# Optimization experiments

Measured on AMD Instinct MI355X. Metric: run time of the kernel, lower is better.

Reference implementation:

```python
import jax, jax.numpy as jnp
from jax import lax
import numpy as np

N_SEG = 8
C_IN = 256
C_RED = C_IN // 16
FOLD = C_IN // 8
EPS = 1e-5


def setup_inputs() -> dict:
    key = jax.random.key(0)
    ks = jax.random.split(key, 6)
    x = jax.random.normal(ks[0], (128, C_IN, 28, 28), dtype=jnp.float32)
    # ta_shift depthwise conv1d weight [C, 3], near one-hot init (learnable)
    w = np.zeros((C_IN, 3), dtype=np.float32)
    w[:FOLD, 2] = 1.0          # shift left (future)
    w[FOLD:2 * FOLD, 0] = 1.0  # shift right (past)
    w[2 * FOLD:, 1] = 1.0      # identity
    ta_shift_w = jnp.asarray(w)
    se_conv_w = jax.random.normal(ks[1], (C_RED, C_IN, 3), dtype=jnp.float32) * (1.0 / np.sqrt(3 * C_IN))
    bn_gamma = jnp.ones((C_RED,), dtype=jnp.float32)
    bn_beta = jnp.zeros((C_RED,), dtype=jnp.float32)
    se_conv1_w = jax.random.normal(ks[2], (C_IN, C_RED), dtype=jnp.float32) * (1.0 / np.sqrt(C_RED))
    net_w = jax.random.normal(ks[3], (C_IN, C_IN, 3, 3), dtype=jnp.float32) * (1.0 / np.sqrt(9 * C_IN))
    net_b = jnp.zeros((C_IN,), dtype=jnp.float32)
    return {"x": x, "ta_shift_w": ta_shift_w, "se_conv_w": se_conv_w,
            "bn_gamma": bn_gamma, "bn_beta": bn_beta, "se_conv1_w": se_conv1_w,
            "net_w": net_w, "net_b": net_b}


def reference(x, ta_shift_w, se_conv_w, bn_gamma, bn_beta, se_conv1_w, net_w, net_b):
    NT, C, H, W = x.shape
    T = N_SEG
    B = NT // T
    # --- temporal shift: depthwise conv1d (k=3, pad=1) over the segment axis ---
    x5 = x.reshape(B, T, C, H, W)
    xp = jnp.pad(x5, ((0, 0), (1, 1), (0, 0), (0, 0), (0, 0)))
    w0 = ta_shift_w[:, 0][None, None, :, None, None]
    w1 = ta_shift_w[:, 1][None, None, :, None, None]
    w2 = ta_shift_w[:, 2][None, None, :, None, None]
    xs = w0 * xp[:, :-2] + w1 * xp[:, 1:-1] + w2 * xp[:, 2:]  # [B,T,C,H,W]
    x_shift = xs.reshape(NT, C, H, W)
    # --- SE-style gating over pooled features ---
    y = x_shift.mean(axis=(2, 3))          # [NT, C]
    # faithful to torch: .view(-1, c, n_segment) reinterprets memory row-major
    y = y.reshape(B, C, T)                 # [B, C, T]
    y = lax.conv_general_dilated(y, se_conv_w, window_strides=(1,),
                                 padding=((1, 1),),
                                 dimension_numbers=("NCH", "OIH", "NCH"))  # [B, C/16, T]
    # BatchNorm1d (training-mode batch statistics over (N, L) per channel)
    mean = y.mean(axis=(0, 2), keepdims=True)
    var = ((y - mean) ** 2).mean(axis=(0, 2), keepdims=True)
    y = (y - mean) * lax.rsqrt(var + EPS)
    y = y * bn_gamma[None, :, None] + bn_beta[None, :, None]
    y = jax.nn.relu(y)
    y = jnp.einsum("oc,bct->bot", se_conv1_w, y)  # 1x1 conv, [B, C, T]
    y = jax.nn.sigmoid(y)
    y = y.reshape(NT, C, 1, 1)             # faithful row-major view back
    z = x_shift + x_shift * y
    # --- wrapped dense conv (self.net) ---
    out = lax.conv_general_dilated(z, net_w, window_strides=(1, 1),
                                   padding=((1, 1), (1, 1)),
                                   dimension_numbers=("NCHW", "OIHW", "NCHW"))
    out = out + net_b[None, :, None, None]
    return out
```

## Files before the change

### kernel.cpp

```cpp
#include <hip/hip_runtime.h>
#include <hip/hip_bf16.h>

typedef unsigned short u16;
typedef short bf16x8 __attribute__((ext_vector_type(8)));
typedef float f32x4 __attribute__((ext_vector_type(4)));
typedef unsigned short u16x8 __attribute__((ext_vector_type(8)));
typedef unsigned short u16x4 __attribute__((ext_vector_type(4)));

#define HW 784
#define PLANE 200704
#define PADPX 900

#define OFF_PX   0
#define OFF_Y3   131072
#define OFF_GL   262144
#define OFF_WT   393216
#define OFF_XSTG 1572864

__device__ __forceinline__ u16 f2b(float f) {
    union { float f; unsigned u; } v; v.f = f;
    unsigned r = v.u + 0x7FFF + ((v.u >> 16) & 1);
    return (u16)(r >> 16);
}

typedef __attribute__((address_space(1))) const unsigned int gas_u32;
typedef __attribute__((address_space(3))) unsigned int las_u32;
__device__ __forceinline__ void gload16(const void* g, void* l) {
    __builtin_amdgcn_global_load_lds((gas_u32*)g, (las_u32*)l, 16, 0, 0);
}

__global__ __launch_bounds__(256) void k_prep(const float* __restrict__ netw, u16* __restrict__ wt,
                                              u16* __restrict__ xstg,
                                              const float* __restrict__ x, float* __restrict__ px) {
    const int bx = blockIdx.x, tid = threadIdx.x;
    if (bx < 2304) {
        int id = bx * 256 + tid;
        int cl = id & 31, co = (id >> 5) & 255, cb = (id >> 13) & 7, tap = id >> 16;
        int ci = cb * 32 + cl;
        wt[id] = f2b(netw[((size_t)co * 256 + ci) * 9 + tap]);
    } else if (bx < 2432) {
        const int nt = bx - 2304;
        for (int it = 0; it < 15; ++it) {
            int cid = it * 256 + tid;
            if (cid < 3712) {
                int pxi = cid >> 5, ch = cid & 31;
                int pidx;
                if (pxi < 30) pidx = pxi;
                else if (pxi < 60) pidx = 29 * 30 + (pxi - 30);
                else { int k = pxi - 60; pidx = (1 + (k >> 1)) * 30 + (k & 1) * 29; }
                *(u16x8*)(xstg + ((size_t)nt * PADPX + pidx) * 256 + ch * 8) = (u16x8){0,0,0,0,0,0,0,0};
            }
        }
    } else {
        const int idx = bx - 2432;
        const int nt = idx >> 2, cg = idx & 3;
        const int wv = tid >> 6, ln = tid & 63;
        for (int i = 0; i < 16; ++i) {
            int c = cg * 64 + wv * 16 + i;
            const float4* xp = (const float4*)(x + (size_t)nt * PLANE + (size_t)c * HW);
            float s = 0.f;
            for (int k = ln; k < 196; k += 64) { float4 v = xp[k]; s += v.x + v.y + v.z + v.w; }
            #pragma unroll
            for (int o = 32; o; o >>= 1) s += __shfl_xor(s, o);
            if (ln == 0) px[nt * 256 + c] = s * (1.f / 784.f);
        }
    }
}

__global__ __launch_bounds__(256) void k_sea(const float* __restrict__ px,
                                             const float* __restrict__ taw,
                                             const float* __restrict__ wse,
                                             float* __restrict__ y3) {
    const int b = blockIdx.x, tid = threadIdx.x;
    __shared__ float ps_l[2048];
    __shared__ float part[2][128];
    #pragma unroll
    for (int i = 0; i < 8; ++i) {
        int e = i * 256 + tid;
        int ts = e >> 8, c = e & 255;
        int nt = b * 8 + ts;
        float v = taw[c * 3 + 1] * px[nt * 256 + c];
        if (ts > 0) v += taw[c * 3] * px[(nt - 1) * 256 + c];
        if (ts < 7) v += taw[c * 3 + 2] * px[(nt + 1) * 256 + c];
        ps_l[e] = v;
    }
    __syncthreads();
    const int half = tid >> 7;
    const int o = (tid & 127) >> 3, t = tid & 7;
    float acc = 0.f;
    const int c2a = half * 128;
    for (int c2 = c2a; c2 < c2a + 128; ++c2) {
        float w0 = wse[(o * 256 + c2) * 3];
        float w1 = wse[(o * 256 + c2) * 3 + 1];
        float w2 = wse[(o * 256 + c2) * 3 + 2];
        float v = w1 * ps_l[c2 * 8 + t];
        if (t > 0) v += w0 * ps_l[c2 * 8 + t - 1];
        if (t < 7) v += w2 * ps_l[c2 * 8 + t + 1];
        acc += v;
    }
    part[half][o * 8 + t] = acc;
    __syncthreads();
    if (tid < 128) y3[b * 128 + tid] = part[0][tid] + part[1][tid];
}

__global__ __launch_bounds__(256) void k_seb(const float* __restrict__ y3,
                                             const float* __restrict__ gamma,
                                             const float* __restrict__ beta,
                                             const float* __restrict__ w1,
                                             float* __restrict__ gl) {
    const int b = blockIdx.x, tid = threadIdx.x;
    __shared__ float y3_l[2048];
    __shared__ float sc[16], bi[16];
    __shared__ float yb[128];
    for (int i = tid; i < 2048; i += 256) y3_l[i] = y3[i];
    __syncthreads();
    if (tid < 16) {
        float s = 0.f, sq = 0.f;
        for (int i = 0; i < 128; ++i) {
            float v = y3_l[(i >> 3) * 128 + tid * 8 + (i & 7)];
            s += v; sq += v * v;
        }
        float m = s * (1.f / 128.f);
        float var = sq * (1.f / 128.f) - m * m;
        float rs = rsqrtf(var + 1e-5f) * gamma[tid];
        sc[tid] = rs; bi[tid] = beta[tid] - m * rs;
    }
    __syncthreads();
    if (tid < 128) {
        int oo = tid >> 3;
        yb[tid] = fmaxf(y3_l[b * 128 + tid] * sc[oo] + bi[oo], 0.f);
    }
    __syncthreads();
    float w1r[16];
    #pragma unroll
    for (int oo = 0; oo < 16; ++oo) w1r[oo] = w1[tid * 16 + oo];
    #pragma unroll
    for (int t = 0; t < 8; ++t) {
        float a = 0.f;
        #pragma unroll
        for (int oo = 0; oo < 16; ++oo) a += w1r[oo] * yb[oo * 8 + t];
        gl[b * 2048 + tid * 8 + t] = 1.f + 1.f / (1.f + __expf(-a));
    }
}

__global__ __launch_bounds__(256) void k_fused(const float* __restrict__ x,
                                               const float* __restrict__ taw,
                                               const float* __restrict__ gl,
                                               u16* __restrict__ xstg) {
    const int pt = blockIdx.x;
    const int nt = blockIdx.y;
    const int tid = threadIdx.x, wv = tid >> 6, ln = tid & 63;
    const int p0 = pt * 56;
    const int tseg = nt & 7;
    __shared__ float taw_l[768];
    __shared__ float gl_l[256];
    __shared__ __align__(16) u16 xs_l[256 * 60];
    for (int i = tid; i < 768; i += 256) taw_l[i] = taw[i];
    gl_l[tid] = gl[nt * 256 + tid];
    __syncthreads();
    const int g = ln >> 4;
    const int l = ln & 15;
    const bool act = l < 14;
    for (int j = 0; j < 16; ++j) {
        const int c = j * 16 + wv * 4 + g;
        const float w0 = taw_l[c * 3], w1 = taw_l[c * 3 + 1], w2 = taw_l[c * 3 + 2];
        const float gc = gl_l[c];
        const float* xb = x + (size_t)nt * PLANE + (size_t)c * HW + p0;
        float4 v0 = {0, 0, 0, 0}, vm = {0, 0, 0, 0}, vp = {0, 0, 0, 0};
        if (act) {
            v0 = *(const float4*)(xb + l * 4);
            if (w0 != 0.f && tseg > 0) vm = *(const float4*)(xb - PLANE + l * 4);
            if (w2 != 0.f && tseg < 7) vp = *(const float4*)(xb + PLANE + l * 4);
        }
        u16x4 o;
        o[0] = f2b((w0 * vm.x + w1 * v0.x + w2 * vp.x) * gc);
        o[1] = f2b((w0 * vm.y + w1 * v0.y + w2 * vp.y) * gc);
        o[2] = f2b((w0 * vm.z + w1 * v0.z + w2 * vp.z) * gc);
        o[3] = f2b((w0 * vm.w + w1 * v0.w + w2 * vp.w) * gc);
        if (act) *(u16x4*)&xs_l[c * 60 + l * 4] = o;
    }
    __syncthreads();
    for (int k = 0; k < 7; ++k) {
        int id = k * 256 + tid;
        int pp = id >> 5;
        int c0 = (id & 31) * 8;
        u16x8 v;
        #pragma unroll
        for (int i = 0; i < 8; ++i) v[i] = xs_l[(c0 + i) * 60 + pp];
        int gp = p0 + pp;
        int r = gp / 28, cc = gp % 28;
        int pidx = (r + 1) * 30 + (cc + 1);
        *(u16x8*)(xstg + ((size_t)nt * PADPX + pidx) * 256 + c0) = v;
    }
}

__global__ __launch_bounds__(256, 3) void k_conv(const u16* __restrict__ xstg,
                                                 const u16* __restrict__ wt,
                                                 const float* __restrict__ netb,
                                                 float* __restrict__ out) {
    const int pt = blockIdx.x;
    const int mt = blockIdx.y;
    const int nt = blockIdx.z;
    const int tid = threadIdx.x, wv = tid >> 6, ln = tid & 63;
    __shared__ __align__(16) u16 z_l[2][6144];
    const int qg = ln >> 4;
    const int p = ln & 15;
    const int g8 = qg * 8;
    int pb[7];
    #pragma unroll
    for (int nf = 0; nf < 7; ++nf) {
        int n = nf * 16 + p;
        pb[nf] = (n / 28) * 30 + (n % 28);
    }
    f32x4 acc[2][7];
    #pragma unroll
    for (int a = 0; a < 2; ++a)
        #pragma unroll
        for (int b = 0; b < 7; ++b) acc[a][b] = (f32x4){0.f, 0.f, 0.f, 0.f};

    const size_t gbase = ((size_t)nt * PADPX + pt * 120) * 256;
    const int maxpix = 899 - pt * 120;
    int pixl[3], ql[3];
    #pragma unroll
    for (int s = 0; s < 3; ++s) {
        int chunk = (wv * 3 + s) * 64 + ln;
        int px_ = chunk >> 2;
        ql[s] = chunk & 3;
        pixl[s] = px_ < maxpix ? px_ : maxpix;
    }

    auto stage = [&](int cb, int buf) {
        #pragma unroll
        for (int s = 0; s < 3; ++s) {
            const u16* g = xstg + gbase + (size_t)pixl[s] * 256 + cb * 32 + ql[s] * 8;
            gload16(g, &z_l[buf][(wv * 3 + s) * 512]);
        }
    };
    auto aload = [&](int tap, int cb, bf16x8* af) {
        const u16* ab = wt + (((size_t)tap * 8 + cb) * 256 + mt * 128 + wv * 32) * 32;
        af[0] = *(const bf16x8*)(ab + p * 32 + g8);
        af[1] = *(const bf16x8*)(ab + (16 + p) * 32 + g8);
    };

    bf16x8 afc[2], afn[2];
    aload(0, 0, afc);
    stage(0, 0);
    for (int cb = 0; cb < 8; ++cb) {
        asm volatile("s_waitcnt vmcnt(0)");
        __syncthreads();
        if (cb < 7) stage(cb + 1, (cb + 1) & 1);
        const u16* zl = z_l[cb & 1];
        #pragma unroll
        for (int tap = 0; tap < 9; ++tap) {
            if (tap < 8) aload(tap + 1, cb, afn);
            else if (cb < 7) aload(0, cb + 1, afn);
            const int po = (tap / 3) * 30 + (tap % 3);
            #pragma unroll
            for (int nf = 0; nf < 7; ++nf) {
                bf16x8 bf = *(const bf16x8*)&zl[(pb[nf] + po) * 32 + g8];
                acc[0][nf] = __builtin_amdgcn_mfma_f32_16x16x32_bf16(afc[0], bf, acc[0][nf], 0, 0, 0);
                acc[1][nf] = __builtin_amdgcn_mfma_f32_16x16x32_bf16(afc[1], bf, acc[1][nf], 0, 0, 0);
            }
            afc[0] = afn[0]; afc[1] = afn[1];
        }
    }
    const int colp = ln & 15, rowp = (ln >> 4) * 4;
    const int o0 = pt * 112;
    #pragma unroll
    for (int mf = 0; mf < 2; ++mf) {
        #pragma unroll
        for (int i = 0; i < 4; ++i) {
            int co = mt * 128 + wv * 32 + mf * 16 + rowp + i;
            float bias = netb[co];
            float* ob = out + ((size_t)nt * 256 + co) * HW + o0;
            #pragma unroll
            for (int nf = 0; nf < 7; ++nf)
                ob[nf * 16 + colp] = acc[mf][nf][i] + bias;
        }
    }
}

extern "C" void kernel_launch(void* const* d_in, const int* in_sizes, int n_in,
                              void* d_out, int out_size, void* d_ws, size_t ws_size,
                              hipStream_t stream) {
    const float* x     = (const float*)d_in[0];
    const float* taw   = (const float*)d_in[1];
    const float* wse   = (const float*)d_in[2];
    const float* gamma = (const float*)d_in[3];
    const float* beta  = (const float*)d_in[4];
    const float* w1    = (const float*)d_in[5];
    const float* netw  = (const float*)d_in[6];
    const float* netb  = (const float*)d_in[7];
    float* out = (float*)d_out;
    char* ws = (char*)d_ws;
    float* px   = (float*)(ws + OFF_PX);
    float* y3   = (float*)(ws + OFF_Y3);
    float* gl   = (float*)(ws + OFF_GL);
    u16*   wt   = (u16*)(ws + OFF_WT);
    u16*   xstg = (u16*)(ws + OFF_XSTG);

    k_prep<<<dim3(2944), dim3(256), 0, stream>>>(netw, wt, xstg, x, px);
    k_sea<<<dim3(16), dim3(256), 0, stream>>>(px, taw, wse, y3);
    k_seb<<<dim3(16), dim3(256), 0, stream>>>(y3, gamma, beta, w1, gl);
    k_fused<<<dim3(14, 128), dim3(256), 0, stream>>>(x, taw, gl, xstg);
    k_conv<<<dim3(7, 2, 128), dim3(256), 0, stream>>>(xstg, wt, netb, out);
}
```

Baseline: 224.8 us.

## Switch conv to 32x32x16 MFMA with full-Cout blocks over two-row tiles

```diff
diff --git a/kernel.cpp b/kernel.cpp
--- a/kernel.cpp
+++ b/kernel.cpp
@@ -4,6 +4,7 @@
 typedef unsigned short u16;
 typedef short bf16x8 __attribute__((ext_vector_type(8)));
 typedef float f32x4 __attribute__((ext_vector_type(4)));
+typedef float f32x16 __attribute__((ext_vector_type(16)));
 typedef unsigned short u16x8 __attribute__((ext_vector_type(8)));
 typedef unsigned short u16x4 __attribute__((ext_vector_type(4)));
 
@@ -199,50 +200,48 @@
                                                  const float* __restrict__ netb,
                                                  float* __restrict__ out) {
     const int pt = blockIdx.x;
-    const int mt = blockIdx.y;
-    const int nt = blockIdx.z;
+    const int nt = blockIdx.y;
     const int tid = threadIdx.x, wv = tid >> 6, ln = tid & 63;
-    __shared__ __align__(16) u16 z_l[2][6144];
-    const int qg = ln >> 4;
-    const int p = ln & 15;
-    const int g8 = qg * 8;
-    int pb[7];
-    #pragma unroll
-    for (int nf = 0; nf < 7; ++nf) {
-        int n = nf * 16 + p;
-        pb[nf] = (n / 28) * 30 + (n % 28);
-    }
-    f32x4 acc[2][7];
+    __shared__ __align__(16) u16 z_l[2][4096];
+    const int lo = ln & 31, hi = ln >> 5;
+    int pb[2];
+    {
+        int n0 = lo;
+        pb[0] = (n0 / 28) * 30 + (n0 % 28);
+        int n1 = 32 + lo; if (n1 > 55) n1 = 55;
+        pb[1] = (n1 / 28) * 30 + (n1 % 28);
+    }
+    const bool val1 = lo < 24;
+    f32x16 acc[2][2];
     #pragma unroll
     for (int a = 0; a < 2; ++a)
         #pragma unroll
-        for (int b = 0; b < 7; ++b) acc[a][b] = (f32x4){0.f, 0.f, 0.f, 0.f};
-
-    const size_t gbase = ((size_t)nt * PADPX + pt * 120) * 256;
-    const int maxpix = 899 - pt * 120;
-    int pixl[3], ql[3];
-    #pragma unroll
-    for (int s = 0; s < 3; ++s) {
-        int chunk = (wv * 3 + s) * 64 + ln;
-        int px_ = chunk >> 2;
-        ql[s] = chunk & 3;
-        pixl[s] = px_ < maxpix ? px_ : maxpix;
-    }
+        for (int b = 0; b < 2; ++b)
+            #pragma unroll
+            for (int i = 0; i < 16; ++i) acc[a][b][i] = 0.f;
+
+    const size_t gb = ((size_t)nt * PADPX + pt * 60) * 256;
 
     auto stage = [&](int cb, int buf) {
         #pragma unroll
-        for (int s = 0; s < 3; ++s) {
-            const u16* g = xstg + gbase + (size_t)pixl[s] * 256 + cb * 32 + ql[s] * 8;
-            gload16(g, &z_l[buf][(wv * 3 + s) * 512]);
+        for (int s = 0; s < 2; ++s) {
+            int chunk = wv * 128 + s * 64 + ln;
+            int pix = chunk >> 2; if (pix > 119) pix = 119;
+            int q = chunk & 3;
+            const u16* g = xstg + gb + (size_t)pix * 256 + cb * 32 + q * 8;
+            gload16(g, &z_l[buf][(wv * 128 + s * 64) * 8]);
         }
     };
     auto aload = [&](int tap, int cb, bf16x8* af) {
-        const u16* ab = wt + (((size_t)tap * 8 + cb) * 256 + mt * 128 + wv * 32) * 32;
-        af[0] = *(const bf16x8*)(ab + p * 32 + g8);
-        af[1] = *(const bf16x8*)(ab + (16 + p) * 32 + g8);
+        const u16* ab = wt + (((size_t)tap * 8 + cb) * 256 + wv * 64) * 32;
+        #pragma unroll
+        for (int mf = 0; mf < 2; ++mf)
+            #pragma unroll
+            for (int kh = 0; kh < 2; ++kh)
+                af[mf * 2 + kh] = *(const bf16x8*)(ab + (mf * 32 + lo) * 32 + kh * 16 + hi * 8);
     };
 
-    bf16x8 afc[2], afn[2];
+    bf16x8 afc[4], afn[4];
     aload(0, 0, afc);
     stage(0, 0);
     for (int cb = 0; cb < 8; ++cb) {
@@ -256,26 +255,28 @@
             else if (cb < 7) aload(0, cb + 1, afn);
             const int po = (tap / 3) * 30 + (tap % 3);
             #pragma unroll
-            for (int nf = 0; nf < 7; ++nf) {
-                bf16x8 bf = *(const bf16x8*)&zl[(pb[nf] + po) * 32 + g8];
-                acc[0][nf] = __builtin_amdgcn_mfma_f32_16x16x32_bf16(afc[0], bf, acc[0][nf], 0, 0, 0);
-                acc[1][nf] = __builtin_amdgcn_mfma_f32_16x16x32_bf16(afc[1], bf, acc[1][nf], 0, 0, 0);
+            for (int j = 0; j < 2; ++j) {
+                #pragma unroll
+                for (int kh = 0; kh < 2; ++kh) {
+                    bf16x8 bf = *(const bf16x8*)&zl[(pb[j] + po) * 32 + kh * 16 + hi * 8];
+                    acc[0][j] = __builtin_amdgcn_mfma_f32_32x32x16_bf16(afc[kh], bf, acc[0][j], 0, 0, 0);
+                    acc[1][j] = __builtin_amdgcn_mfma_f32_32x32x16_bf16(afc[2 + kh], bf, acc[1][j], 0, 0, 0);
+                }
             }
-            afc[0] = afn[0]; afc[1] = afn[1];
-        }
-    }
-    const int colp = ln & 15, rowp = (ln >> 4) * 4;
-    const int o0 = pt * 112;
+            #pragma unroll
+            for (int q2 = 0; q2 < 4; ++q2) afc[q2] = afn[q2];
+        }
+    }
+    const int p0 = pt * 56;
     #pragma unroll
     for (int mf = 0; mf < 2; ++mf) {
         #pragma unroll
-        for (int i = 0; i < 4; ++i) {
-            int co = mt * 128 + wv * 32 + mf * 16 + rowp + i;
+        for (int i = 0; i < 16; ++i) {
+            int co = wv * 64 + mf * 32 + (i & 3) + 8 * (i >> 2) + 4 * hi;
             float bias = netb[co];
-            float* ob = out + ((size_t)nt * 256 + co) * HW + o0;
-            #pragma unroll
-            for (int nf = 0; nf < 7; ++nf)
-                ob[nf * 16 + colp] = acc[mf][nf][i] + bias;
+            float* ob = out + ((size_t)nt * 256 + co) * HW + p0;
+            ob[lo] = acc[mf][0][i] + bias;
+            if (val1) ob[32 + lo] = acc[mf][1][i] + bias;
         }
     }
 }
@@ -303,5 +304,5 @@
     k_sea<<<dim3(16), dim3(256), 0, stream>>>(px, taw, wse, y3);
     k_seb<<<dim3(16), dim3(256), 0, stream>>>(y3, gamma, beta, w1, gl);
     k_fused<<<dim3(14, 128), dim3(256), 0, stream>>>(x, taw, gl, xstg);
-    k_conv<<<dim3(7, 2, 128), dim3(256), 0, stream>>>(xstg, wt, netb, out);
-}
+    k_conv<<<dim3(14, 128), dim3(256), 0, stream>>>(xstg, wt, netb, out);
+}
```

Result: slower. 272.6 us (+21.2%).
